# Kernel tuning notes

Measured on AMD Instinct MI355X. Metric: run time of the kernel, lower is better.

## Reference

```python
import jax, jax.numpy as jnp
import numpy as np

N = 100_000   # nodes
E = 3_200_000 # edges (avg degree 32)
F_NODE = 64
F_EDGE = 16
HID = 64
NEG_SLOPE = 0.2


def _gat_conv(x, src, dst, edge_attr, W, a_src, a_dst, We, a_e, bias, n):
    """PyG GATConv (heads=1, edge_dim, add_self_loops=True fill='mean', eval mode)."""
    # --- add self loops; loop edge_attr = mean of incoming edge_attr per node ---
    deg = jax.ops.segment_sum(jnp.ones((src.shape[0],), x.dtype), dst, num_segments=n)
    loop_attr = jax.ops.segment_sum(edge_attr, dst, num_segments=n)
    loop_attr = jnp.where(deg[:, None] > 0, loop_attr / jnp.maximum(deg, 1.0)[:, None], 0.0)
    loop = jnp.arange(n, dtype=src.dtype)
    src2 = jnp.concatenate([src, loop])
    dst2 = jnp.concatenate([dst, loop])
    ea = jnp.concatenate([edge_attr, loop_attr], axis=0)

    # --- node / edge projections and per-node attention terms ---
    h = x @ W                                   # [N, HID]
    alpha_src = h @ a_src                       # [N]
    alpha_dst = h @ a_dst                       # [N]
    e = ea @ We                                 # [E+N, HID]
    alpha_e = e @ a_e                           # [E+N]

    # --- per-edge logits + segment softmax over destination neighborhoods ---
    logits = jax.nn.leaky_relu(alpha_src[src2] + alpha_dst[dst2] + alpha_e, NEG_SLOPE)
    seg_max = jax.ops.segment_max(logits, dst2, num_segments=n)  # every node has self loop
    ex = jnp.exp(logits - seg_max[dst2])
    denom = jax.ops.segment_sum(ex, dst2, num_segments=n)
    w = ex / denom[dst2]                        # [E+N]

    # --- weighted scatter-aggregate of messages ---
    out = jax.ops.segment_sum(h[src2] * w[:, None], dst2, num_segments=n)
    return out + bias


def setup_inputs() -> dict:
    key = jax.random.key(0)
    ks = jax.random.split(key, 16)
    s = 0.1  # keep logits tame
    return {
        "x": jax.random.normal(ks[0], (N, F_NODE), jnp.float32),
        "edge_index": jax.random.randint(ks[1], (2, E), 0, N, jnp.int32),
        "edge_attr": jax.random.normal(ks[2], (E, F_EDGE), jnp.float32),
        "W1": jax.random.normal(ks[3], (F_NODE, HID), jnp.float32) * s,
        "att_src1": jax.random.normal(ks[4], (HID,), jnp.float32) * s,
        "att_dst1": jax.random.normal(ks[5], (HID,), jnp.float32) * s,
        "We1": jax.random.normal(ks[6], (F_EDGE, HID), jnp.float32) * s,
        "att_edge1": jax.random.normal(ks[7], (HID,), jnp.float32) * s,
        "b1": jnp.zeros((HID,), jnp.float32),
        "W2": jax.random.normal(ks[8], (HID, HID), jnp.float32) * s,
        "att_src2": jax.random.normal(ks[9], (HID,), jnp.float32) * s,
        "att_dst2": jax.random.normal(ks[10], (HID,), jnp.float32) * s,
        "We2": jax.random.normal(ks[11], (F_EDGE, HID), jnp.float32) * s,
        "att_edge2": jax.random.normal(ks[12], (HID,), jnp.float32) * s,
        "b2": jnp.zeros((HID,), jnp.float32),
        "fc_w": jax.random.normal(ks[13], (HID, 1), jnp.float32) * s,
        "fc_b": jnp.zeros((1,), jnp.float32),
    }


def reference(x, edge_index, edge_attr, W1, att_src1, att_dst1, We1, att_edge1, b1,
              W2, att_src2, att_dst2, We2, att_edge2, b2, fc_w, fc_b):
    src, dst = edge_index[0], edge_index[1]
    n = x.shape[0]
    h = jax.nn.elu(_gat_conv(x, src, dst, edge_attr, W1, att_src1, att_dst1, We1, att_edge1, b1, n))
    h = jax.nn.elu(_gat_conv(h, src, dst, edge_attr, W2, att_src2, att_dst2, We2, att_edge2, b2, n))
    return h @ fc_w + fc_b  # [N, 1] logits
```

## Files before the change

kernel.cpp:

```cpp
#include <hip/hip_runtime.h>
#include <hip/hip_bf16.h>
#include <hip/hip_fp16.h>
#include <math.h>
#include <stdint.h>

constexpr int HIDDIM = 64;
constexpr int FEDGE  = 16;
constexpr int BN     = 256;
constexpr int CAP    = 9216;
constexpr int TILE   = 2048;
constexpr int NTA    = 512;
constexpr int EPT    = TILE / NTA;

__global__ void compute_c_kernel(const float* __restrict__ We1, const float* __restrict__ ae1,
                                 const float* __restrict__ We2, const float* __restrict__ ae2,
                                 float* __restrict__ c) {
  int t = threadIdx.x;
  if (t < FEDGE) {
    float s = 0.f;
    for (int j = 0; j < HIDDIM; ++j) s += We1[t * HIDDIM + j] * ae1[j];
    c[t] = s;
  } else if (t < 2 * FEDGE) {
    int k = t - FEDGE;
    float s = 0.f;
    for (int j = 0; j < HIDDIM; ++j) s += We2[k * HIDDIM + j] * ae2[j];
    c[FEDGE + k] = s;
  }
}

__global__ __launch_bounds__(256) void edgefeat_kernel(
    const float* __restrict__ attr, const float* __restrict__ c,
    float2* __restrict__ a12, int E) {
  __shared__ float cs[32];
  if (threadIdx.x < 32) cs[threadIdx.x] = c[threadIdx.x];
  __syncthreads();
  int lane = threadIdx.x & 63;
  int wid  = threadIdx.x >> 6;
  int q = lane & 3;
  int g = lane >> 2;
  const float4* attr4 = (const float4*)attr;
  int wavesTotal = (blockDim.x >> 6) * gridDim.x;
  int waveId = blockIdx.x * (blockDim.x >> 6) + wid;
  for (long long base = (long long)waveId * 16; base < E; base += (long long)wavesTotal * 16) {
    int e = (int)base + g;
    float4 v = make_float4(0.f, 0.f, 0.f, 0.f);
    if (e < E) v = attr4[(size_t)e * 4 + q];
    float a1 = v.x * cs[4*q]    + v.y * cs[4*q+1]    + v.z * cs[4*q+2]    + v.w * cs[4*q+3];
    float a2 = v.x * cs[16+4*q] + v.y * cs[16+4*q+1] + v.z * cs[16+4*q+2] + v.w * cs[16+4*q+3];
    a1 += __shfl_xor(a1, 1, 64); a1 += __shfl_xor(a1, 2, 64);
    a2 += __shfl_xor(a2, 1, 64); a2 += __shfl_xor(a2, 2, 64);
    if (q == 0 && e < E) a12[e] = make_float2(a1, a2);
  }
}

__global__ __launch_bounds__(NTA) void passA_kernel(
    const int* __restrict__ src, const int* __restrict__ dst,
    const float2* __restrict__ a12,
    int* __restrict__ bucketCursor, float4* __restrict__ P, int E, int nbuck) {
  __shared__ int s_rx[TILE];
  __shared__ int s_ry[TILE];
  __shared__ int s_rz[TILE];
  __shared__ int s_rw[TILE];
  __shared__ int cnt[400];
  __shared__ int lbase[512];
  __shared__ int gbase[400];
  for (int i = threadIdx.x; i < nbuck; i += NTA) cnt[i] = 0;
  __syncthreads();
  int e0 = blockIdx.x * TILE;
  int tileCnt = min(TILE, E - e0);

  int d_reg[EPT];
#pragma unroll
  for (int k = 0; k < EPT; ++k) {
    int e = e0 + k * NTA + threadIdx.x;
    d_reg[k] = (e < E) ? dst[e] : -1;
  }
#pragma unroll
  for (int k = 0; k < EPT; ++k) {
    if (d_reg[k] >= 0) atomicAdd(&cnt[d_reg[k] >> 8], 1);
  }
  __syncthreads();

  {
    int t = threadIdx.x;
    int v = (t < nbuck) ? cnt[t] : 0;
    lbase[t] = v;
    __syncthreads();
    for (int d = 1; d < 512; d <<= 1) {
      int tv = (t >= d) ? lbase[t - d] : 0;
      __syncthreads();
      lbase[t] += tv;
      __syncthreads();
    }
    lbase[t] -= v;
  }
  for (int i = threadIdx.x; i < nbuck; i += NTA) {
    int n = cnt[i];
    gbase[i] = (n > 0) ? atomicAdd(&bucketCursor[i], n) : 0;
    cnt[i] = 0;
  }
  __syncthreads();

#pragma unroll
  for (int k = 0; k < EPT; ++k) {
    int d = d_reg[k];
    if (d < 0) continue;
    int e = e0 + k * NTA + threadIdx.x;
    int b = d >> 8;
    float2 a = a12[e];
    int sE = src[e];
    int r = atomicAdd(&cnt[b], 1);
    int idx = lbase[b] + r;
    s_rx[idx] = sE;
    s_ry[idx] = __float_as_int(a.x);
    s_rz[idx] = __float_as_int(a.y);
    s_rw[idx] = d;
  }
  __syncthreads();

  for (int i = threadIdx.x; i < tileCnt; i += NTA) {
    int d = s_rw[i];
    int b = d >> 8;
    int rank = i - lbase[b];
    int pos = gbase[b] + rank;
    if (pos < CAP) {
      float4 o;
      o.x = __int_as_float(s_rx[i]);
      o.y = __int_as_float(s_ry[i]);
      o.z = __int_as_float(s_rz[i]);
      o.w = __int_as_float(d);
      P[(size_t)b * CAP + pos] = o;
    }
  }
}

__global__ void scan_buckets_kernel(const int* __restrict__ bucketCursor,
                                    int* __restrict__ bucketBase,
                                    int* __restrict__ offsets, int nbuck, int N, int E) {
  __shared__ int s[512];
  int t = threadIdx.x;
  int v = (t < nbuck) ? min(bucketCursor[t], CAP) : 0;
  s[t] = v;
  __syncthreads();
  for (int d = 1; d < 512; d <<= 1) {
    int tv = (t >= d) ? s[t - d] : 0;
    __syncthreads();
    s[t] += tv;
    __syncthreads();
  }
  if (t < nbuck) bucketBase[t] = s[t] - v;
  if (t == 0) offsets[N] = E;
}

__global__ __launch_bounds__(256) void passB_kernel(
    const float4* __restrict__ P, const int* __restrict__ bucketCursor,
    const int* __restrict__ bucketBase, int* __restrict__ offsets,
    float2* __restrict__ EDG1, float2* __restrict__ EDG2, int N) {
  int b = blockIdx.x;
  int t = threadIdx.x;
  int nodeBase = b * BN;
  int cnt = min(bucketCursor[b], CAP);
  int gbase = bucketBase[b];
  __shared__ int hist[BN];
  __shared__ int cur[BN];
  __shared__ int wsum[4];
  hist[t] = 0;
  __syncthreads();
  const float4* Pb = P + (size_t)b * CAP;
  for (int i = t; i < cnt; i += 256) {
    int d = __float_as_int(Pb[i].w);
    atomicAdd(&hist[d - nodeBase], 1);
  }
  __syncthreads();
  int deg = hist[t];
  int lane = t & 63, wid = t >> 6;
  int incl = deg;
#pragma unroll
  for (int d = 1; d < 64; d <<= 1) {
    int tv = __shfl_up(incl, d, 64);
    if (lane >= d) incl += tv;
  }
  if (lane == 63) wsum[wid] = incl;
  __syncthreads();
  int woff = 0;
  for (int w = 0; w < wid; ++w) woff += wsum[w];
  int excl = incl - deg + woff;
  int nodeId = nodeBase + t;
  if (nodeId < N) offsets[nodeId] = gbase + excl;
  cur[t] = gbase + excl;
  __syncthreads();
  for (int i = t; i < cnt; i += 256) {
    float4 r = Pb[i];
    int d = __float_as_int(r.w);
    int pos = atomicAdd(&cur[d - nodeBase], 1);
    EDG1[pos] = make_float2(r.x, r.y);
    EDG2[pos] = make_float2(r.x, r.z);
  }
}

__global__ __launch_bounds__(256) void gemm_alpha_kernel(
    const float* __restrict__ X, const float* __restrict__ W,
    const float* __restrict__ a_src, const float* __restrict__ a_dst,
    __half2* __restrict__ H, float* __restrict__ alpha_s, float* __restrict__ alpha_d, int n) {
  __shared__ float Ws[HIDDIM * HIDDIM];
  __shared__ float as_s[HIDDIM], ad_s[HIDDIM];
  for (int i = threadIdx.x; i < HIDDIM * HIDDIM; i += blockDim.x) Ws[i] = W[i];
  if (threadIdx.x < HIDDIM) {
    as_s[threadIdx.x] = a_src[threadIdx.x];
    ad_s[threadIdx.x] = a_dst[threadIdx.x];
  }
  __syncthreads();
  int lane = threadIdx.x & 63;
  int wid  = threadIdx.x >> 6;
  int wavesTotal = (blockDim.x >> 6) * gridDim.x;
  for (int row = blockIdx.x * (blockDim.x >> 6) + wid; row < n; row += wavesTotal) {
    float xv = X[(size_t)row * HIDDIM + lane];
    float acc = 0.f;
#pragma unroll
    for (int k = 0; k < HIDDIM; ++k) {
      float xk = __shfl(xv, k, 64);
      acc = fmaf(xk, Ws[k * HIDDIM + lane], acc);
    }
    float accN = __shfl_xor(acc, 1, 64);
    if (!(lane & 1)) {
      H[(size_t)row * 32 + (lane >> 1)] = __floats2half2_rn(acc, accN);
    }
    float s1 = acc * as_s[lane];
    float s2 = acc * ad_s[lane];
#pragma unroll
    for (int d = 32; d > 0; d >>= 1) {
      s1 += __shfl_xor(s1, d, 64);
      s2 += __shfl_xor(s2, d, 64);
    }
    if (lane == 0) {
      alpha_s[row] = s1;
      alpha_d[row] = s2;
    }
  }
}

__device__ __forceinline__ float leaky(float x) { return (x < 0.f) ? 0.2f * x : x; }
__device__ __forceinline__ float elu(float x) { return (x > 0.f) ? x : (__expf(x) - 1.f); }

template <bool FINAL>
__global__ __launch_bounds__(256) void aggregate_kernel(
    const __half2* __restrict__ H, const float* __restrict__ alpha_s, const float* __restrict__ alpha_d,
    const float2* __restrict__ EDG, const int* __restrict__ offsets,
    const float* __restrict__ bias, const float* __restrict__ fc_w, const float* __restrict__ fc_b,
    float* __restrict__ out, int n) {
  int lane = threadIdx.x & 63;
  int wid  = threadIdx.x >> 6;
  int node = blockIdx.x * (blockDim.x >> 6) + wid;
  if (node >= n) return;
  int off = offsets[node];
  int deg = offsets[node + 1] - off;
  float ad  = alpha_d[node];
  float asn = alpha_s[node];

  if (deg <= 64) {
    float2 ed = make_float2(0.f, 0.f);
    if (lane < deg) ed = EDG[off + lane];
    int   s_l  = __float_as_int(ed.x);
    float ae_l = ed.y;
    float as_g = (lane < deg) ? alpha_s[s_l] : 0.f;
    float lg_l = (lane < deg) ? leaky(as_g + ad + ae_l) : -INFINITY;
    float aesum = (lane < deg) ? ae_l : 0.f;
    float lmax = lg_l;
#pragma unroll
    for (int d = 32; d > 0; d >>= 1) {
      lmax = fmaxf(lmax, __shfl_xor(lmax, d, 64));
      aesum += __shfl_xor(aesum, d, 64);
    }
    float self_ae = (deg > 0) ? aesum / (float)deg : 0.f;
    float slg = leaky(asn + ad + self_ae);
    float m = fmaxf(lmax, slg);

    float ex_l = (lane < deg) ? __expf(lg_l - m) : 0.f;
    float dsum = ex_l;
#pragma unroll
    for (int d = 32; d > 0; d >>= 1) dsum += __shfl_xor(dsum, d, 64);
    float exs = __expf(slg - m);
    float denom = dsum + exs;

    int half = lane >> 5;
    int c32  = lane & 31;

    float selfw = (half == 0) ? exs : 0.f;
    float2 hv = __half22float2(H[(size_t)node * 32 + c32]);
    float2 acc2;
    acc2.x = selfw * hv.x;
    acc2.y = selfw * hv.y;

    int jj = 0;
    for (; jj + 16 <= deg; jj += 16) {
      int   si[8]; float ei[8];
#pragma unroll
      for (int k = 0; k < 8; ++k) {
        si[k] = __shfl(s_l, jj + 2 * k + half, 64);
        ei[k] = __shfl(ex_l, jj + 2 * k + half, 64);
      }
      float2 hh[8];
#pragma unroll
      for (int k = 0; k < 8; ++k) hh[k] = __half22float2(H[(size_t)si[k] * 32 + c32]);
#pragma unroll
      for (int k = 0; k < 8; ++k) {
        acc2.x = fmaf(ei[k], hh[k].x, acc2.x);
        acc2.y = fmaf(ei[k], hh[k].y, acc2.y);
      }
    }
    for (; jj + 8 <= deg; jj += 8) {
      int j0 = jj + half, j1 = jj + 2 + half, j2 = jj + 4 + half, j3 = jj + 6 + half;
      int   sa = __shfl(s_l, j0, 64),  sb = __shfl(s_l, j1, 64);
      int   sc = __shfl(s_l, j2, 64),  sd = __shfl(s_l, j3, 64);
      float ea = __shfl(ex_l, j0, 64), eb = __shfl(ex_l, j1, 64);
      float ec = __shfl(ex_l, j2, 64), ef = __shfl(ex_l, j3, 64);
      float2 ha = __half22float2(H[(size_t)sa * 32 + c32]);
      float2 hb = __half22float2(H[(size_t)sb * 32 + c32]);
      float2 hc = __half22float2(H[(size_t)sc * 32 + c32]);
      float2 hd = __half22float2(H[(size_t)sd * 32 + c32]);
      acc2.x = fmaf(ea, ha.x, acc2.x); acc2.y = fmaf(ea, ha.y, acc2.y);
      acc2.x = fmaf(eb, hb.x, acc2.x); acc2.y = fmaf(eb, hb.y, acc2.y);
      acc2.x = fmaf(ec, hc.x, acc2.x); acc2.y = fmaf(ec, hc.y, acc2.y);
      acc2.x = fmaf(ef, hd.x, acc2.x); acc2.y = fmaf(ef, hd.y, acc2.y);
    }
    for (; jj < deg; jj += 2) {
      int j = jj + half;
      int   sj = __shfl(s_l, j, 64);
      float ej = __shfl(ex_l, j, 64);
      float2 hj = __half22float2(H[(size_t)sj * 32 + c32]);
      acc2.x = fmaf(ej, hj.x, acc2.x);
      acc2.y = fmaf(ej, hj.y, acc2.y);
    }
    acc2.x += __shfl_xor(acc2.x, 32, 64);
    acc2.y += __shfl_xor(acc2.y, 32, 64);

    const float2* bi2 = (const float2*)bias;
    float2 bv = bi2[c32];
    float rx = elu(acc2.x / denom + bv.x);
    float ry = elu(acc2.y / denom + bv.y);
    if (!FINAL) {
      if (half == 0) {
        float2 o; o.x = rx; o.y = ry;
        ((float2*)out)[(size_t)node * 32 + c32] = o;
      }
    } else {
      const float2* fw2 = (const float2*)fc_w;
      float2 fv = fw2[c32];
      float s1 = rx * fv.x + ry * fv.y;
#pragma unroll
      for (int d = 16; d > 0; d >>= 1) s1 += __shfl_xor(s1, d, 64);
      if (lane == 0) out[node] = s1 + fc_b[0];
    }
    return;
  }

  {
    const __half* Hh = (const __half*)H;
    float lmax = -INFINITY, aesum = 0.f;
    for (int base = 0; base < deg; base += 64) {
      int i = base + lane;
      if (i < deg) {
        float2 ed = EDG[off + i];
        int s = __float_as_int(ed.x);
        float ae = ed.y;
        float lg = leaky(alpha_s[s] + ad + ae);
        lmax = fmaxf(lmax, lg);
        aesum += ae;
      }
    }
#pragma unroll
    for (int d = 32; d > 0; d >>= 1) {
      lmax = fmaxf(lmax, __shfl_xor(lmax, d, 64));
      aesum += __shfl_xor(aesum, d, 64);
    }
    float self_ae = aesum / (float)deg;
    float slg = leaky(asn + ad + self_ae);
    float m = fmaxf(lmax, slg);
    float exs = __expf(slg - m);
    float dsum = 0.f;
    float acc = exs * __half2float(Hh[(size_t)node * HIDDIM + lane]);
    for (int base = 0; base < deg; base += 64) {
      int i = base + lane;
      int cnt = min(64, deg - base);
      float2 ed = make_float2(0.f, 0.f);
      if (i < deg) ed = EDG[off + i];
      int   s_l  = __float_as_int(ed.x);
      float ae_l = ed.y;
      float ex_l = (lane < cnt) ? __expf(leaky(alpha_s[s_l] + ad + ae_l) - m) : 0.f;
      dsum += ex_l;
      for (int j = 0; j < cnt; ++j) {
        int   sj = __shfl(s_l, j, 64);
        float ej = __shfl(ex_l, j, 64);
        acc = fmaf(ej, __half2float(Hh[(size_t)sj * HIDDIM + lane]), acc);
      }
    }
#pragma unroll
    for (int d = 32; d > 0; d >>= 1) dsum += __shfl_xor(dsum, d, 64);
    float denom = dsum + exs;

    float res = elu(acc / denom + bias[lane]);
    if (!FINAL) {
      out[(size_t)node * HIDDIM + lane] = res;
    } else {
      float s1 = res * fc_w[lane];
#pragma unroll
      for (int d = 32; d > 0; d >>= 1) s1 += __shfl_xor(s1, d, 64);
      if (lane == 0) out[node] = s1 + fc_b[0];
    }
  }
}

extern "C" void kernel_launch(void* const* d_in, const int* in_sizes, int n_in,
                              void* d_out, int out_size, void* d_ws, size_t ws_size,
                              hipStream_t stream) {
  const float* x    = (const float*)d_in[0];
  const int*   ei   = (const int*)d_in[1];
  const float* attr = (const float*)d_in[2];
  const float* W1   = (const float*)d_in[3];
  const float* as1  = (const float*)d_in[4];
  const float* ad1  = (const float*)d_in[5];
  const float* We1  = (const float*)d_in[6];
  const float* ae1  = (const float*)d_in[7];
  const float* b1   = (const float*)d_in[8];
  const float* W2   = (const float*)d_in[9];
  const float* as2  = (const float*)d_in[10];
  const float* ad2  = (const float*)d_in[11];
  const float* We2  = (const float*)d_in[12];
  const float* ae2  = (const float*)d_in[13];
  const float* b2   = (const float*)d_in[14];
  const float* fcw  = (const float*)d_in[15];
  const float* fcb  = (const float*)d_in[16];

  const int N = in_sizes[0] / HIDDIM;
  const int E = in_sizes[1] / 2;
  const int NBUCK = (N + BN - 1) / BN;

  char* p = (char*)d_ws;
  auto alloc = [&](size_t bytes) -> void* {
    void* r = (void*)p;
    p += (bytes + 255) & ~(size_t)255;
    return r;
  };
  float*  c            = (float*)alloc(32 * sizeof(float));
  int*    bucketCursor = (int*)alloc((size_t)NBUCK * 4);
  int*    bucketBase   = (int*)alloc(((size_t)NBUCK + 1) * 4);
  int*    offsets      = (int*)alloc(((size_t)N + 1) * 4);
  float*  alpha_s      = (float*)alloc((size_t)N * 4);
  float*  alpha_d      = (float*)alloc((size_t)N * 4);
  float2* EDG1         = (float2*)alloc((size_t)E * 8);
  float2* EDG2         = (float2*)alloc((size_t)E * 8);
  size_t  regionBytes  = (size_t)NBUCK * CAP * 16;
  size_t  hBytes       = (size_t)N * HIDDIM * 2;
  size_t  x2Bytes      = (size_t)N * HIDDIM * 4;
  if (hBytes + x2Bytes > regionBytes) regionBytes = hBytes + x2Bytes;
  char*   region       = (char*)alloc(regionBytes);
  float4* P            = (float4*)region;
  __half2* H           = (__half2*)region;
  float*  X2           = (float*)(region + ((hBytes + 255) & ~(size_t)255));

  float2* a12 = EDG1;

  const int* srcp = ei;
  const int* dstp = ei + E;

  hipMemsetAsync(bucketCursor, 0, (size_t)NBUCK * 4, stream);

  compute_c_kernel<<<1, 64, 0, stream>>>(We1, ae1, We2, ae2, c);
  edgefeat_kernel<<<2048, 256, 0, stream>>>(attr, c, a12, E);

  int ablocks = (E + TILE - 1) / TILE;
  passA_kernel<<<ablocks, NTA, 0, stream>>>(srcp, dstp, a12, bucketCursor, P, E, NBUCK);
  scan_buckets_kernel<<<1, 512, 0, stream>>>(bucketCursor, bucketBase, offsets, NBUCK, N, E);
  passB_kernel<<<NBUCK, 256, 0, stream>>>(P, bucketCursor, bucketBase, offsets, EDG1, EDG2, N);

  int aggBlocks = (N + 3) / 4;

  gemm_alpha_kernel<<<2048, 256, 0, stream>>>(x, W1, as1, ad1, H, alpha_s, alpha_d, N);
  aggregate_kernel<false><<<aggBlocks, 256, 0, stream>>>(H, alpha_s, alpha_d, EDG1,
                                                         offsets, b1, nullptr, nullptr, X2, N);
  gemm_alpha_kernel<<<2048, 256, 0, stream>>>(X2, W2, as2, ad2, H, alpha_s, alpha_d, N);
  aggregate_kernel<true><<<aggBlocks, 256, 0, stream>>>(H, alpha_s, alpha_d, EDG2,
                                                        offsets, b2, fcw, fcb, (float*)d_out, N);
}
```

Before: 493.5 us.

## Fuse edge-feature projection into bucketing pass and pack edge records compactly

The separate edgefeat kernel is removed and its per-edge attention projection is computed inside passA straight from edge_attr. The two per-layer edge terms are packed as fp16 pair into one int, and the local destination index is packed into the source index word, so bucket records shrink from 16 to 8 bytes. passB writes a single shared int2 edge array instead of two float2 arrays, and both aggregate layers read it with a template selector. This cuts global traffic in the preprocessing and scatter stages at the cost of fp16 precision on the edge logits and a 20-bit limit on node ids.

```diff
diff --git a/kernel.cpp b/kernel.cpp
--- a/kernel.cpp
+++ b/kernel.cpp
@@ -28,42 +28,30 @@
   }
 }
 
-__global__ __launch_bounds__(256) void edgefeat_kernel(
-    const float* __restrict__ attr, const float* __restrict__ c,
-    float2* __restrict__ a12, int E) {
-  __shared__ float cs[32];
-  if (threadIdx.x < 32) cs[threadIdx.x] = c[threadIdx.x];
-  __syncthreads();
-  int lane = threadIdx.x & 63;
-  int wid  = threadIdx.x >> 6;
-  int q = lane & 3;
-  int g = lane >> 2;
-  const float4* attr4 = (const float4*)attr;
-  int wavesTotal = (blockDim.x >> 6) * gridDim.x;
-  int waveId = blockIdx.x * (blockDim.x >> 6) + wid;
-  for (long long base = (long long)waveId * 16; base < E; base += (long long)wavesTotal * 16) {
-    int e = (int)base + g;
-    float4 v = make_float4(0.f, 0.f, 0.f, 0.f);
-    if (e < E) v = attr4[(size_t)e * 4 + q];
-    float a1 = v.x * cs[4*q]    + v.y * cs[4*q+1]    + v.z * cs[4*q+2]    + v.w * cs[4*q+3];
-    float a2 = v.x * cs[16+4*q] + v.y * cs[16+4*q+1] + v.z * cs[16+4*q+2] + v.w * cs[16+4*q+3];
-    a1 += __shfl_xor(a1, 1, 64); a1 += __shfl_xor(a1, 2, 64);
-    a2 += __shfl_xor(a2, 1, 64); a2 += __shfl_xor(a2, 2, 64);
-    if (q == 0 && e < E) a12[e] = make_float2(a1, a2);
-  }
+__device__ __forceinline__ int pack_ae(float a1, float a2) {
+  unsigned lo = __half_as_ushort(__float2half_rn(a1));
+  unsigned hi = __half_as_ushort(__float2half_rn(a2));
+  return (int)((hi << 16) | lo);
+}
+template <int SEL>
+__device__ __forceinline__ float unpack_ae(int pk) {
+  unsigned u = (SEL == 0) ? ((unsigned)pk & 0xFFFFu) : ((unsigned)pk >> 16);
+  return __half2float(__ushort_as_half((unsigned short)u));
 }
 
 __global__ __launch_bounds__(NTA) void passA_kernel(
     const int* __restrict__ src, const int* __restrict__ dst,
-    const float2* __restrict__ a12,
-    int* __restrict__ bucketCursor, float4* __restrict__ P, int E, int nbuck) {
-  __shared__ int s_rx[TILE];
-  __shared__ int s_ry[TILE];
-  __shared__ int s_rz[TILE];
-  __shared__ int s_rw[TILE];
+    const float* __restrict__ attr, const float* __restrict__ c,
+    int* __restrict__ bucketCursor, int2* __restrict__ P, int E, int nbuck) {
+  __shared__ int st_ae[TILE];
+  __shared__ int s_key[TILE];
+  __shared__ int s_ae[TILE];
+  __shared__ int s_b[TILE];
   __shared__ int cnt[400];
   __shared__ int lbase[512];
   __shared__ int gbase[400];
+  __shared__ float cs[32];
+  if (threadIdx.x < 32) cs[threadIdx.x] = c[threadIdx.x];
   for (int i = threadIdx.x; i < nbuck; i += NTA) cnt[i] = 0;
   __syncthreads();
   int e0 = blockIdx.x * TILE;
@@ -78,6 +66,24 @@
 #pragma unroll
   for (int k = 0; k < EPT; ++k) {
     if (d_reg[k] >= 0) atomicAdd(&cnt[d_reg[k] >> 8], 1);
+  }
+
+  {
+    int q   = threadIdx.x & 3;
+    int grp = threadIdx.x >> 2;
+    const float4* attr4 = (const float4*)attr;
+#pragma unroll
+    for (int pass = 0; pass < TILE / 128; ++pass) {
+      int el = pass * 128 + grp;
+      int e = e0 + el;
+      float4 v = make_float4(0.f, 0.f, 0.f, 0.f);
+      if (e < E) v = attr4[(size_t)e * 4 + q];
+      float a1 = v.x * cs[4*q]    + v.y * cs[4*q+1]    + v.z * cs[4*q+2]    + v.w * cs[4*q+3];
+      float a2 = v.x * cs[16+4*q] + v.y * cs[16+4*q+1] + v.z * cs[16+4*q+2] + v.w * cs[16+4*q+3];
+      a1 += __shfl_xor(a1, 1, 64); a1 += __shfl_xor(a1, 2, 64);
+      a2 += __shfl_xor(a2, 1, 64); a2 += __shfl_xor(a2, 2, 64);
+      if (q == 0) st_ae[el] = pack_ae(a1, a2);
+    }
   }
   __syncthreads();
 
@@ -105,32 +111,23 @@
   for (int k = 0; k < EPT; ++k) {
     int d = d_reg[k];
     if (d < 0) continue;
-    int e = e0 + k * NTA + threadIdx.x;
+    int el = k * NTA + threadIdx.x;
+    int e = e0 + el;
     int b = d >> 8;
-    float2 a = a12[e];
     int sE = src[e];
     int r = atomicAdd(&cnt[b], 1);
     int idx = lbase[b] + r;
-    s_rx[idx] = sE;
-    s_ry[idx] = __float_as_int(a.x);
-    s_rz[idx] = __float_as_int(a.y);
-    s_rw[idx] = d;
+    s_key[idx] = sE | ((d & 255) << 20);
+    s_ae[idx]  = st_ae[el];
+    s_b[idx]   = b;
   }
   __syncthreads();
 
   for (int i = threadIdx.x; i < tileCnt; i += NTA) {
-    int d = s_rw[i];
-    int b = d >> 8;
+    int b = s_b[i];
     int rank = i - lbase[b];
     int pos = gbase[b] + rank;
-    if (pos < CAP) {
-      float4 o;
-      o.x = __int_as_float(s_rx[i]);
-      o.y = __int_as_float(s_ry[i]);
-      o.z = __int_as_float(s_rz[i]);
-      o.w = __int_as_float(d);
-      P[(size_t)b * CAP + pos] = o;
-    }
+    if (pos < CAP) P[(size_t)b * CAP + pos] = make_int2(s_key[i], s_ae[i]);
   }
 }
 
@@ -153,9 +150,9 @@
 }
 
 __global__ __launch_bounds__(256) void passB_kernel(
-    const float4* __restrict__ P, const int* __restrict__ bucketCursor,
+    const int2* __restrict__ P, const int* __restrict__ bucketCursor,
     const int* __restrict__ bucketBase, int* __restrict__ offsets,
-    float2* __restrict__ EDG1, float2* __restrict__ EDG2, int N) {
+    int2* __restrict__ EDGS, int N) {
   int b = blockIdx.x;
   int t = threadIdx.x;
   int nodeBase = b * BN;
@@ -166,10 +163,10 @@
   __shared__ int wsum[4];
   hist[t] = 0;
   __syncthreads();
-  const float4* Pb = P + (size_t)b * CAP;
+  const int2* Pb = P + (size_t)b * CAP;
   for (int i = t; i < cnt; i += 256) {
-    int d = __float_as_int(Pb[i].w);
-    atomicAdd(&hist[d - nodeBase], 1);
+    int dl = (Pb[i].x >> 20) & 255;
+    atomicAdd(&hist[dl], 1);
   }
   __syncthreads();
   int deg = hist[t];
@@ -190,11 +187,10 @@
   cur[t] = gbase + excl;
   __syncthreads();
   for (int i = t; i < cnt; i += 256) {
-    float4 r = Pb[i];
-    int d = __float_as_int(r.w);
-    int pos = atomicAdd(&cur[d - nodeBase], 1);
-    EDG1[pos] = make_float2(r.x, r.y);
-    EDG2[pos] = make_float2(r.x, r.z);
+    int2 r = Pb[i];
+    int dl = (r.x >> 20) & 255;
+    int pos = atomicAdd(&cur[dl], 1);
+    EDGS[pos] = r;
   }
 }
 
@@ -242,10 +238,10 @@
 __device__ __forceinline__ float leaky(float x) { return (x < 0.f) ? 0.2f * x : x; }
 __device__ __forceinline__ float elu(float x) { return (x > 0.f) ? x : (__expf(x) - 1.f); }
 
-template <bool FINAL>
+template <bool FINAL, int SEL>
 __global__ __launch_bounds__(256) void aggregate_kernel(
     const __half2* __restrict__ H, const float* __restrict__ alpha_s, const float* __restrict__ alpha_d,
-    const float2* __restrict__ EDG, const int* __restrict__ offsets,
+    const int2* __restrict__ EDGS, const int* __restrict__ offsets,
     const float* __restrict__ bias, const float* __restrict__ fc_w, const float* __restrict__ fc_b,
     float* __restrict__ out, int n) {
   int lane = threadIdx.x & 63;
@@ -258,10 +254,10 @@
   float asn = alpha_s[node];
 
   if (deg <= 64) {
-    float2 ed = make_float2(0.f, 0.f);
-    if (lane < deg) ed = EDG[off + lane];
-    int   s_l  = __float_as_int(ed.x);
-    float ae_l = ed.y;
+    int2 ed = make_int2(0, 0);
+    if (lane < deg) ed = EDGS[off + lane];
+    int   s_l  = ed.x & 0xFFFFF;
+    float ae_l = unpack_ae<SEL>(ed.y);
     float as_g = (lane < deg) ? alpha_s[s_l] : 0.f;
     float lg_l = (lane < deg) ? leaky(as_g + ad + ae_l) : -INFINITY;
     float aesum = (lane < deg) ? ae_l : 0.f;
@@ -360,9 +356,9 @@
     for (int base = 0; base < deg; base += 64) {
       int i = base + lane;
       if (i < deg) {
-        float2 ed = EDG[off + i];
-        int s = __float_as_int(ed.x);
-        float ae = ed.y;
+        int2 ed = EDGS[off + i];
+        int s = ed.x & 0xFFFFF;
+        float ae = unpack_ae<SEL>(ed.y);
         float lg = leaky(alpha_s[s] + ad + ae);
         lmax = fmaxf(lmax, lg);
         aesum += ae;
@@ -382,10 +378,10 @@
     for (int base = 0; base < deg; base += 64) {
       int i = base + lane;
       int cnt = min(64, deg - base);
-      float2 ed = make_float2(0.f, 0.f);
-      if (i < deg) ed = EDG[off + i];
-      int   s_l  = __float_as_int(ed.x);
-      float ae_l = ed.y;
+      int2 ed = make_int2(0, 0);
+      if (i < deg) ed = EDGS[off + i];
+      int   s_l  = ed.x & 0xFFFFF;
+      float ae_l = unpack_ae<SEL>(ed.y);
       float ex_l = (lane < cnt) ? __expf(leaky(alpha_s[s_l] + ad + ae_l) - m) : 0.f;
       dsum += ex_l;
       for (int j = 0; j < cnt; ++j) {
@@ -447,38 +443,34 @@
   int*    offsets      = (int*)alloc(((size_t)N + 1) * 4);
   float*  alpha_s      = (float*)alloc((size_t)N * 4);
   float*  alpha_d      = (float*)alloc((size_t)N * 4);
-  float2* EDG1         = (float2*)alloc((size_t)E * 8);
-  float2* EDG2         = (float2*)alloc((size_t)E * 8);
-  size_t  regionBytes  = (size_t)NBUCK * CAP * 16;
+  int2*   EDGS         = (int2*)alloc((size_t)E * 8);
+  size_t  regionBytes  = (size_t)NBUCK * CAP * 8;
   size_t  hBytes       = (size_t)N * HIDDIM * 2;
   size_t  x2Bytes      = (size_t)N * HIDDIM * 4;
   if (hBytes + x2Bytes > regionBytes) regionBytes = hBytes + x2Bytes;
   char*   region       = (char*)alloc(regionBytes);
-  float4* P            = (float4*)region;
+  int2*   P            = (int2*)region;
   __half2* H           = (__half2*)region;
   float*  X2           = (float*)(region + ((hBytes + 255) & ~(size_t)255));
 
-  float2* a12 = EDG1;
-
   const int* srcp = ei;
   const int* dstp = ei + E;
 
   hipMemsetAsync(bucketCursor, 0, (size_t)NBUCK * 4, stream);
 
   compute_c_kernel<<<1, 64, 0, stream>>>(We1, ae1, We2, ae2, c);
-  edgefeat_kernel<<<2048, 256, 0, stream>>>(attr, c, a12, E);
 
   int ablocks = (E + TILE - 1) / TILE;
-  passA_kernel<<<ablocks, NTA, 0, stream>>>(srcp, dstp, a12, bucketCursor, P, E, NBUCK);
+  passA_kernel<<<ablocks, NTA, 0, stream>>>(srcp, dstp, attr, c, bucketCursor, P, E, NBUCK);
   scan_buckets_kernel<<<1, 512, 0, stream>>>(bucketCursor, bucketBase, offsets, NBUCK, N, E);
-  passB_kernel<<<NBUCK, 256, 0, stream>>>(P, bucketCursor, bucketBase, offsets, EDG1, EDG2, N);
+  passB_kernel<<<NBUCK, 256, 0, stream>>>(P, bucketCursor, bucketBase, offsets, EDGS, N);
 
   int aggBlocks = (N + 3) / 4;
 
   gemm_alpha_kernel<<<2048, 256, 0, stream>>>(x, W1, as1, ad1, H, alpha_s, alpha_d, N);
-  aggregate_kernel<false><<<aggBlocks, 256, 0, stream>>>(H, alpha_s, alpha_d, EDG1,
-                                                         offsets, b1, nullptr, nullptr, X2, N);
+  aggregate_kernel<false, 0><<<aggBlocks, 256, 0, stream>>>(H, alpha_s, alpha_d, EDGS,
+                                                            offsets, b1, nullptr, nullptr, X2, N);
   gemm_alpha_kernel<<<2048, 256, 0, stream>>>(X2, W2, as2, ad2, H, alpha_s, alpha_d, N);
-  aggregate_kernel<true><<<aggBlocks, 256, 0, stream>>>(H, alpha_s, alpha_d, EDG2,
-                                                        offsets, b2, fcw, fcb, (float*)d_out, N);
-}
+  aggregate_kernel<true, 1><<<aggBlocks, 256, 0, stream>>>(H, alpha_s, alpha_d, EDGS,
+                                                           offsets, b2, fcw, fcb, (float*)d_out, N);
+}
```

After: 449.9 us. -8.8%, faster.
